# Kernel optimization log

Hardware: AMD Instinct MI355X
Metric: run time of the kernel (lower is better)

## Reference

```python
import jax, jax.numpy as jnp
import numpy as np

TAU = 2.0        # LIF membrane time constant
VTH = 0.5        # spike threshold
EPS = 1e-5       # BatchNorm eps
ALPHA = 2.0      # ATan surrogate alpha (spikingjelly default)


@jax.custom_vjp
def atan_heaviside(x):
    # forward: Heaviside spike; backward: ATan surrogate gradient
    return (x >= 0.0).astype(x.dtype)

def _ah_fwd(x):
    return atan_heaviside(x), x

def _ah_bwd(x, g):
    return (g * (ALPHA / 2.0) / (1.0 + (jnp.pi / 2.0 * ALPHA * x) ** 2),)

atan_heaviside.defvjp(_ah_fwd, _ah_bwd)


def lif_multistep(x):
    # x: [T, ...] -> spikes [T, ...]; hard reset to 0, decay_input=True
    def step(v, xt):
        v = v + (xt - v) / TAU
        s = atan_heaviside(v - VTH)
        v = v * (1.0 - jax.lax.stop_gradient(s))  # detach_reset=True
        return v, s
    v0 = jnp.zeros_like(x[0])
    _, spikes = jax.lax.scan(step, v0, x)
    return spikes


def tape_pe(d_model, max_len, dtype):
    # tAPE (ConvTran): sinusoidal PE with d_model/max_len frequency scaling
    pos = jnp.arange(max_len, dtype=dtype)[:, None]
    div = jnp.exp(jnp.arange(0, d_model, 2, dtype=dtype) * (-np.log(10000.0) / d_model))
    arg = pos * div * (d_model / max_len)
    pe = jnp.zeros((max_len, d_model), dtype)
    pe = pe.at[:, 0::2].set(jnp.sin(arg))
    pe = pe.at[:, 1::2].set(jnp.cos(arg))
    return pe  # [N, D]


def setup_inputs() -> dict:
    key = jax.random.key(0)
    k1, k2 = jax.random.split(key)
    T, B, N, P, D = 4, 64, 196, 768, 256
    x = jax.random.normal(k1, (T, B, N, P), dtype=jnp.float32)
    W = jax.random.normal(k2, (D, P), dtype=jnp.float32) * 0.02
    gamma = jnp.ones((D,), dtype=jnp.float32)
    beta = jnp.zeros((D,), dtype=jnp.float32)
    return {"x": x, "W": W, "gamma": gamma, "beta": beta}


def reference(x, W, gamma, beta):
    T, B, N, P = x.shape
    D = W.shape[0]
    # patch linear (no bias): [T,B,N,P] @ [D,P]^T -> [T,B,N,D]
    h = jnp.einsum('tbnp,dp->tbnd', x, W)
    h = jnp.transpose(h, (0, 1, 3, 2))  # [T,B,D,N]
    # BatchNorm1d over channel D (training-mode batch stats over T*B and N)
    mean = h.mean(axis=(0, 1, 3), keepdims=True)
    var = ((h - mean) ** 2).mean(axis=(0, 1, 3), keepdims=True)
    h = (h - mean) * jax.lax.rsqrt(var + EPS)
    h = h * gamma[None, None, :, None] + beta[None, None, :, None]
    # LIF spiking neuron scan over T
    h = lif_multistep(h)
    # tAPE positional encoding (broadcast [D,N] over T,B) + second LIF
    h = h + tape_pe(D, N, h.dtype).T
    h = lif_multistep(h)
    return jnp.transpose(h, (0, 1, 3, 2))  # [T,B,N,D]
```

## Files before the change

kernel.cpp:

```cpp
#include <hip/hip_runtime.h>
#include <cmath>

#define T_    4
#define B_    64
#define N_    196
#define P_    768
#define D_    256
#define BN_   (B_*N_)
#define M_    (T_*BN_)
#define SITES (BN_*D_)

#define TILE  64
#define TK    16
#define KITER (P_/TK)
#define MBLKS (M_/TILE)
#define NBLKS (D_/TILE)
#define RLEN  98

typedef __attribute__((ext_vector_type(2))) float f32x2;

__device__ __forceinline__ void pk_fma(f32x2& acc, f32x2 a, f32x2 b) {
    f32x2 t;
    asm("v_pk_mul_f32 %1, %2, %3\n\t"
        "v_pk_add_f32 %0, %0, %1"
        : "+v"(acc), "=&v"(t) : "v"(a), "v"(b));
}

extern "C" __global__ __launch_bounds__(256)
void gemm_f32emu(const float* __restrict__ x, const float* __restrict__ w,
                 float* __restrict__ h, float* __restrict__ hT) {
    __shared__ __align__(16) f32x2 As2[2][TK/2][RLEN];
    __shared__ __align__(16) f32x2 Bs2[2][TK/2][RLEN];

    const int tid  = threadIdx.x;
    const int tx   = tid & 15;
    const int ty   = tid >> 4;
    const int bid  = blockIdx.x;
    const int xcd  = bid & 7;
    const int lin  = bid >> 3;
    const int m0   = (xcd * 98 + (lin >> 2)) * TILE;
    const int d0   = (lin & 3) * TILE;
    const int lrow = tid >> 2;
    const int kq   = tid & 3;
    const int lk   = kq * 4;
    const int woff = (lrow >> 2) * 6 + (lrow & 3);
    const int abase = ty * 6;
    const int bbase = tx * 6;

    const float* xp = x + (size_t)(m0 + lrow) * P_ + lk;
    const float* wp = w + (size_t)(d0 + lrow) * P_ + lk;

    f32x2 acc[4][4][2];
#pragma unroll
    for (int i = 0; i < 4; ++i)
#pragma unroll
        for (int j = 0; j < 4; ++j)
#pragma unroll
            for (int p = 0; p < 2; ++p) acc[i][j][p] = f32x2{0.0f, 0.0f};

    {
        const float4 av = *(const float4*)xp;
        const float4 bv = *(const float4*)wp;
        As2[0][kq * 2 + 0][woff] = f32x2{av.x, av.y};
        As2[0][kq * 2 + 1][woff] = f32x2{av.z, av.w};
        Bs2[0][kq * 2 + 0][woff] = f32x2{bv.x, bv.y};
        Bs2[0][kq * 2 + 1][woff] = f32x2{bv.z, bv.w};
    }

    int cur = 0;
    for (int k0 = 0; k0 < KITER; ++k0) {
        __syncthreads();
        float4 av, bv;
        const bool have = (k0 + 1 < KITER);
        if (have) {
            av = *(const float4*)(xp + (k0 + 1) * TK);
            bv = *(const float4*)(wp + (k0 + 1) * TK);
        }
#pragma unroll
        for (int kp = 0; kp < TK / 2; ++kp) {
            const int pi = kp & 1;
            const f32x2* Ar = As2[cur][kp];
            const f32x2* Br = Bs2[cur][kp];
            const float4 aa0 = *(const float4*)(Ar + abase);
            const float4 aa1 = *(const float4*)(Ar + abase + 2);
            const float4 bb0 = *(const float4*)(Br + bbase);
            const float4 bb1 = *(const float4*)(Br + bbase + 2);
            f32x2 a2[4], b2[4];
            a2[0] = f32x2{aa0.x, aa0.y}; a2[1] = f32x2{aa0.z, aa0.w};
            a2[2] = f32x2{aa1.x, aa1.y}; a2[3] = f32x2{aa1.z, aa1.w};
            b2[0] = f32x2{bb0.x, bb0.y}; b2[1] = f32x2{bb0.z, bb0.w};
            b2[2] = f32x2{bb1.x, bb1.y}; b2[3] = f32x2{bb1.z, bb1.w};
#pragma unroll
            for (int i = 0; i < 4; ++i)
#pragma unroll
                for (int j = 0; j < 4; ++j)
                    pk_fma(acc[i][j][pi], a2[i], b2[j]);
        }
        if (have) {
            As2[cur ^ 1][kq * 2 + 0][woff] = f32x2{av.x, av.y};
            As2[cur ^ 1][kq * 2 + 1][woff] = f32x2{av.z, av.w};
            Bs2[cur ^ 1][kq * 2 + 0][woff] = f32x2{bv.x, bv.y};
            Bs2[cur ^ 1][kq * 2 + 1][woff] = f32x2{bv.z, bv.w};
        }
        cur ^= 1;
    }

    float res[4][4];
#pragma unroll
    for (int i = 0; i < 4; ++i)
#pragma unroll
        for (int j = 0; j < 4; ++j) {
            const float l01 = __fadd_rn(acc[i][j][0].x, acc[i][j][0].y);
            const float l23 = __fadd_rn(acc[i][j][1].x, acc[i][j][1].y);
            res[i][j] = __fadd_rn(l01, l23);
        }
#pragma unroll
    for (int i = 0; i < 4; ++i) {
        float4 o = {res[i][0], res[i][1], res[i][2], res[i][3]};
        *(float4*)(h + (size_t)(m0 + ty * 4 + i) * D_ + d0 + tx * 4) = o;
    }
    if (hT) {
#pragma unroll
        for (int j = 0; j < 4; ++j) {
            float4 o = {res[0][j], res[1][j], res[2][j], res[3][j]};
            *(float4*)(hT + (size_t)(d0 + tx * 4 + j) * M_ + m0 + ty * 4) = o;
        }
    }
}

#define MCH2 7168
#define GRP  224
extern "C" __global__ __launch_bounds__(256)
void mean_hT(const float* __restrict__ hT, float* __restrict__ mean_) {
    __shared__ float buf[2][MCH2];
    const int tid = threadIdx.x;
    const float* src = hT + (size_t)blockIdx.x * M_;

#pragma unroll
    for (int u = 0; u < 7; ++u)
        *(float4*)&buf[0][(u * 256 + tid) * 4] =
            *(const float4*)&src[(u * 256 + tid) * 4];
    __syncthreads();

    float acc = 0.0f;
    for (int c = 0; c < 7; ++c) {
        const int cb = c & 1;
        const bool have = (c + 1 < 7);
        float4 v[7];
        if (have) {
            const float* rp = src + (c + 1) * MCH2;
#pragma unroll
            for (int u = 0; u < 7; ++u)
                v[u] = *(const float4*)&rp[(u * 256 + tid) * 4];
        }
        if (tid == 0) {
            const float4* bp = (const float4*)buf[cb];
            float4 p0[8], p1[8];
#pragma unroll
            for (int u = 0; u < 8; ++u) p0[u] = bp[u];
            for (int gp = 0; gp < GRP; gp += 2) {
#pragma unroll
                for (int u = 0; u < 8; ++u) p1[u] = bp[(gp + 1) * 8 + u];
#pragma unroll
                for (int u = 0; u < 8; ++u) {
                    acc = __fadd_rn(acc, p0[u].x);
                    acc = __fadd_rn(acc, p0[u].y);
                    acc = __fadd_rn(acc, p0[u].z);
                    acc = __fadd_rn(acc, p0[u].w);
                }
                const int g2 = (gp + 2 < GRP) ? gp + 2 : 0;
#pragma unroll
                for (int u = 0; u < 8; ++u) p0[u] = bp[g2 * 8 + u];
#pragma unroll
                for (int u = 0; u < 8; ++u) {
                    acc = __fadd_rn(acc, p1[u].x);
                    acc = __fadd_rn(acc, p1[u].y);
                    acc = __fadd_rn(acc, p1[u].z);
                    acc = __fadd_rn(acc, p1[u].w);
                }
            }
        }
        if (have) {
#pragma unroll
            for (int u = 0; u < 7; ++u)
                *(float4*)&buf[cb ^ 1][(u * 256 + tid) * 4] = v[u];
        }
        __syncthreads();
    }
    if (tid == 0) mean_[blockIdx.x] = __fdiv_rn(acc, 50176.0f);
}

extern "C" __global__ __launch_bounds__(256)
void var_hT(const float* __restrict__ hT, const float* __restrict__ mean_,
            float* __restrict__ inv_) {
    __shared__ float chunks[256];
    const int d    = blockIdx.x;
    const int tid  = threadIdx.x;
    const int wv   = tid >> 6;
    const int lane = tid & 63;
    const float mn = mean_[d];
    const float* col = hT + (size_t)d * M_;

    for (int tb = wv; tb < T_ * B_; tb += 4) {
        double part = 0.0;
        for (int n = lane; n < N_; n += 64) {
            const float hv = col[tb * N_ + n];
            const float t1 = __fsub_rn(hv, mn);
            const float sq = __fmul_rn(t1, t1);
            part += (double)sq;
        }
#pragma unroll
        for (int off = 32; off; off >>= 1) part += __shfl_down(part, off);
        if (lane == 0) chunks[tb] = (float)part;
    }
    __syncthreads();
    if (tid == 0) {
        float accf = 0.0f;
        for (int tb = 0; tb < T_ * B_; ++tb) accf = __fadd_rn(accf, chunks[tb]);
        const float var = __fdiv_rn(accf, 50176.0f);
        inv_[d] = __fdiv_rn(1.0f, __fsqrt_rn(__fadd_rn(var, 1e-5f)));
    }
}

#define MCH  256
#define DCH  16
#define PADW 20
#define NCHK (M_/MCH)

extern "C" __global__ __launch_bounds__(256)
void mean_seq(const float* __restrict__ h, float* __restrict__ mean_) {
    __shared__ __align__(16) float buf[2][MCH][PADW];
    const int tid = threadIdx.x;
    const int d0  = blockIdx.x * DCH;
    {
        const float* rp = h + (size_t)tid * D_ + d0;
        *(float4*)&buf[0][tid][0]  = *(const float4*)(rp + 0);
        *(float4*)&buf[0][tid][4]  = *(const float4*)(rp + 4);
        *(float4*)&buf[0][tid][8]  = *(const float4*)(rp + 8);
        *(float4*)&buf[0][tid][12] = *(const float4*)(rp + 12);
    }
    __syncthreads();
    float acc = 0.0f;
    for (int c = 0; c < NCHK; ++c) {
        const int cb = c & 1;
        const bool have = (c + 1 < NCHK);
        float4 v0, v1, v2, v3;
        if (have) {
            const float* rp = h + ((size_t)(c + 1) * MCH + tid) * D_ + d0;
            v0 = *(const float4*)(rp + 0);
            v1 = *(const float4*)(rp + 4);
            v2 = *(const float4*)(rp + 8);
            v3 = *(const float4*)(rp + 12);
        }
        if (tid < DCH) {
#pragma unroll 16
            for (int m = 0; m < MCH; ++m)
                acc = __fadd_rn(acc, buf[cb][m][tid]);
        }
        if (have) {
            *(float4*)&buf[cb ^ 1][tid][0]  = v0;
            *(float4*)&buf[cb ^ 1][tid][4]  = v1;
            *(float4*)&buf[cb ^ 1][tid][8]  = v2;
            *(float4*)&buf[cb ^ 1][tid][12] = v3;
        }
        __syncthreads();
    }
    if (tid < DCH) mean_[d0 + tid] = __fdiv_rn(acc, 50176.0f);
}

extern "C" __global__ __launch_bounds__(64)
void var_seq(const float* __restrict__ h, const float* __restrict__ mean_,
             float* __restrict__ inv_) {
    const int d    = blockIdx.x;
    const int lane = threadIdx.x;
    const float mn = mean_[d];
    float accf = 0.0f;
    for (int tb = 0; tb < T_ * B_; ++tb) {
        double part = 0.0;
        for (int n = lane; n < N_; n += 64) {
            const float hv = h[((size_t)tb * N_ + n) * D_ + d];
            const float t1 = __fsub_rn(hv, mn);
            const float sq = __fmul_rn(t1, t1);
            part += (double)sq;
        }
#pragma unroll
        for (int off = 32; off; off >>= 1) part += __shfl_down(part, off);
        accf = __fadd_rn(accf, (float)part);
    }
    if (lane == 0) {
        const float var = __fdiv_rn(accf, 50176.0f);
        inv_[d] = __fdiv_rn(1.0f, __fsqrt_rn(__fadd_rn(var, 1e-5f)));
    }
}

extern "C" __global__ __launch_bounds__(256)
void pe_build(float* __restrict__ pe_) {
    const int d = threadIdx.x;
    const int n = blockIdx.x;
    const double dv  = exp((double)(d & ~1) * (-9.210340371976184 / 256.0));
    const double arg = ((double)n * dv) * (256.0 / 196.0);
    pe_[(size_t)n * D_ + d] = (d & 1) ? (float)cos(arg) : (float)sin(arg);
}

extern "C" __global__ __launch_bounds__(256)
void lif_final(float* __restrict__ out, const float* __restrict__ mean_,
               const float* __restrict__ inv_, const float* __restrict__ gamma,
               const float* __restrict__ beta, const float* __restrict__ pe_tab) {
    const int idx = blockIdx.x * 256 + threadIdx.x;
    const int d = idx & (D_ - 1);
    const int n = (idx >> 8) % N_;

    const float mn = mean_[d];
    const float iv = inv_[d];
    const float g  = gamma[d];
    const float b  = beta[d];

    float pe;
    if (pe_tab) {
        pe = pe_tab[(size_t)n * D_ + d];
    } else {
        const double dv  = exp((double)(d & ~1) * (-9.210340371976184 / 256.0));
        const double arg = ((double)n * dv) * (256.0 / 196.0);
        pe = (d & 1) ? (float)cos(arg) : (float)sin(arg);
    }

    float hv[4];
#pragma unroll
    for (int t = 0; t < T_; ++t) hv[t] = out[(size_t)t * SITES + idx];

    float v1 = 0.0f, v2 = 0.0f, s2v[4];
#pragma unroll
    for (int t = 0; t < T_; ++t) {
        const float t1 = __fsub_rn(hv[t], mn);
        const float u  = __fmul_rn(t1, iv);
        const float hb = __fadd_rn(__fmul_rn(u, g), b);
        v1 = __fadd_rn(v1, __fmul_rn(__fsub_rn(hb, v1), 0.5f));
        const float s1 = (v1 >= 0.5f) ? 1.0f : 0.0f;
        v1 = __fmul_rn(v1, __fsub_rn(1.0f, s1));
        const float y = __fadd_rn(s1, pe);
        v2 = __fadd_rn(v2, __fmul_rn(__fsub_rn(y, v2), 0.5f));
        const float s2 = (v2 >= 0.5f) ? 1.0f : 0.0f;
        v2 = __fmul_rn(v2, __fsub_rn(1.0f, s2));
        s2v[t] = s2;
    }
#pragma unroll
    for (int t = 0; t < T_; ++t) out[(size_t)t * SITES + idx] = s2v[t];
}

extern "C" void kernel_launch(void* const* d_in, const int* in_sizes, int n_in,
                              void* d_out, int out_size, void* d_ws, size_t ws_size,
                              hipStream_t stream) {
    const float* x     = (const float*)d_in[0];
    const float* w     = (const float*)d_in[1];
    const float* gamma = (const float*)d_in[2];
    const float* beta  = (const float*)d_in[3];
    float* out = (float*)d_out;

    float* mean_ = (float*)d_ws;
    float* inv_  = mean_ + D_;
    float* pe_   = inv_  + D_;
    float* hT_   = pe_   + (size_t)N_ * D_;

    const size_t need_pe = (size_t)(2 * D_ + N_ * D_) * sizeof(float);
    const size_t need_hT = need_pe + (size_t)M_ * D_ * sizeof(float);
    const bool use_pe = ws_size >= need_pe;
    const bool use_hT = ws_size >= need_hT;

    gemm_f32emu<<<MBLKS * NBLKS, 256, 0, stream>>>(x, w, out,
                                                   use_hT ? hT_ : nullptr);
    if (use_hT) {
        mean_hT<<<D_, 256, 0, stream>>>(hT_, mean_);
        var_hT<<<D_, 256, 0, stream>>>(hT_, mean_, inv_);
    } else {
        mean_seq<<<16, 256, 0, stream>>>(out, mean_);
        var_seq<<<D_, 64, 0, stream>>>(out, mean_, inv_);
    }
    if (use_pe) pe_build<<<N_, 256, 0, stream>>>(pe_);
    lif_final<<<SITES / 256, 256, 0, stream>>>(out, mean_, inv_, gamma, beta,
                                               use_pe ? pe_ : nullptr);
}
```

Measured before the change: 855.6 us.

## Split GEMM launch, fuse mean/var reduction, vectorize LIF epilogue

Splits the GEMM grid into two half-launches over M, fuses the mean and variance reduction kernels into one block-per-channel kernel, removes the wraparound prefetch in the serial mean loop, and vectorizes the final LIF kernel to process four channels per thread with float4 loads and stores. The aim is to cut launch overhead and the redundant reread of statistics, and to widen memory transactions in the epilogue. The extra GEMM launch may add tail and launch cost.

```diff
diff --git a/kernel.cpp b/kernel.cpp
--- a/kernel.cpp
+++ b/kernel.cpp
@@ -14,7 +14,8 @@
 #define TK    16
 #define KITER (P_/TK)
 #define MBLKS (M_/TILE)
-#define NBLKS (D_/TILE)
+#define HBLKS (392/49*8*4/8)
+#define GRID_HALF ((392/49)*49*4/4)
 #define RLEN  98
 
 typedef __attribute__((ext_vector_type(2))) float f32x2;
@@ -28,7 +29,7 @@
 
 extern "C" __global__ __launch_bounds__(256)
 void gemm_f32emu(const float* __restrict__ x, const float* __restrict__ w,
-                 float* __restrict__ h, float* __restrict__ hT) {
+                 float* __restrict__ h, float* __restrict__ hT, int mbase) {
     __shared__ __align__(16) f32x2 As2[2][TK/2][RLEN];
     __shared__ __align__(16) f32x2 Bs2[2][TK/2][RLEN];
 
@@ -38,7 +39,7 @@
     const int bid  = blockIdx.x;
     const int xcd  = bid & 7;
     const int lin  = bid >> 3;
-    const int m0   = (xcd * 98 + (lin >> 2)) * TILE;
+    const int m0   = mbase + (xcd * 49 + (lin >> 2)) * TILE;
     const int d0   = (lin & 3) * TILE;
     const int lrow = tid >> 2;
     const int kq   = tid & 3;
@@ -131,10 +132,14 @@
 #define MCH2 7168
 #define GRP  224
 extern "C" __global__ __launch_bounds__(256)
-void mean_hT(const float* __restrict__ hT, float* __restrict__ mean_) {
+void meanvar_hT(const float* __restrict__ hT, float* __restrict__ mean_,
+                float* __restrict__ inv_) {
     __shared__ float buf[2][MCH2];
+    __shared__ float chunks[256];
+    __shared__ float mn_sh;
     const int tid = threadIdx.x;
-    const float* src = hT + (size_t)blockIdx.x * M_;
+    const int d   = blockIdx.x;
+    const float* src = hT + (size_t)d * M_;
 
 #pragma unroll
     for (int u = 0; u < 7; ++u)
@@ -158,7 +163,8 @@
             float4 p0[8], p1[8];
 #pragma unroll
             for (int u = 0; u < 8; ++u) p0[u] = bp[u];
-            for (int gp = 0; gp < GRP; gp += 2) {
+            int gp = 0;
+            for (; gp + 2 < GRP; gp += 2) {
 #pragma unroll
                 for (int u = 0; u < 8; ++u) p1[u] = bp[(gp + 1) * 8 + u];
 #pragma unroll
@@ -168,9 +174,8 @@
                     acc = __fadd_rn(acc, p0[u].z);
                     acc = __fadd_rn(acc, p0[u].w);
                 }
-                const int g2 = (gp + 2 < GRP) ? gp + 2 : 0;
-#pragma unroll
-                for (int u = 0; u < 8; ++u) p0[u] = bp[g2 * 8 + u];
+#pragma unroll
+                for (int u = 0; u < 8; ++u) p0[u] = bp[(gp + 2) * 8 + u];
 #pragma unroll
                 for (int u = 0; u < 8; ++u) {
                     acc = __fadd_rn(acc, p1[u].x);
@@ -179,6 +184,22 @@
                     acc = __fadd_rn(acc, p1[u].w);
                 }
             }
+#pragma unroll
+            for (int u = 0; u < 8; ++u) p1[u] = bp[(GRP - 1) * 8 + u];
+#pragma unroll
+            for (int u = 0; u < 8; ++u) {
+                acc = __fadd_rn(acc, p0[u].x);
+                acc = __fadd_rn(acc, p0[u].y);
+                acc = __fadd_rn(acc, p0[u].z);
+                acc = __fadd_rn(acc, p0[u].w);
+            }
+#pragma unroll
+            for (int u = 0; u < 8; ++u) {
+                acc = __fadd_rn(acc, p1[u].x);
+                acc = __fadd_rn(acc, p1[u].y);
+                acc = __fadd_rn(acc, p1[u].z);
+                acc = __fadd_rn(acc, p1[u].w);
+            }
         }
         if (have) {
 #pragma unroll
@@ -187,24 +208,20 @@
         }
         __syncthreads();
     }
-    if (tid == 0) mean_[blockIdx.x] = __fdiv_rn(acc, 50176.0f);
-}
-
-extern "C" __global__ __launch_bounds__(256)
-void var_hT(const float* __restrict__ hT, const float* __restrict__ mean_,
-            float* __restrict__ inv_) {
-    __shared__ float chunks[256];
-    const int d    = blockIdx.x;
-    const int tid  = threadIdx.x;
+    if (tid == 0) {
+        const float mn = __fdiv_rn(acc, 50176.0f);
+        mean_[d] = mn;
+        mn_sh = mn;
+    }
+    __syncthreads();
+
+    const float mn = mn_sh;
     const int wv   = tid >> 6;
     const int lane = tid & 63;
-    const float mn = mean_[d];
-    const float* col = hT + (size_t)d * M_;
-
     for (int tb = wv; tb < T_ * B_; tb += 4) {
         double part = 0.0;
         for (int n = lane; n < N_; n += 64) {
-            const float hv = col[tb * N_ + n];
+            const float hv = src[tb * N_ + n];
             const float t1 = __fsub_rn(hv, mn);
             const float sq = __fmul_rn(t1, t1);
             part += (double)sq;
@@ -306,45 +323,61 @@
 void lif_final(float* __restrict__ out, const float* __restrict__ mean_,
                const float* __restrict__ inv_, const float* __restrict__ gamma,
                const float* __restrict__ beta, const float* __restrict__ pe_tab) {
-    const int idx = blockIdx.x * 256 + threadIdx.x;
-    const int d = idx & (D_ - 1);
-    const int n = (idx >> 8) % N_;
-
-    const float mn = mean_[d];
-    const float iv = inv_[d];
-    const float g  = gamma[d];
-    const float b  = beta[d];
-
-    float pe;
+    const int base = (blockIdx.x * 256 + threadIdx.x) * 4;
+    const int dbase = base & (D_ - 1);
+    const int n = (base >> 8) % N_;
+
+    const float4 mn = *(const float4*)&mean_[dbase];
+    const float4 iv = *(const float4*)&inv_[dbase];
+    const float4 g  = *(const float4*)&gamma[dbase];
+    const float4 b  = *(const float4*)&beta[dbase];
+
+    float4 pe;
     if (pe_tab) {
-        pe = pe_tab[(size_t)n * D_ + d];
+        pe = *(const float4*)&pe_tab[(size_t)n * D_ + dbase];
     } else {
-        const double dv  = exp((double)(d & ~1) * (-9.210340371976184 / 256.0));
-        const double arg = ((double)n * dv) * (256.0 / 196.0);
-        pe = (d & 1) ? (float)cos(arg) : (float)sin(arg);
-    }
-
-    float hv[4];
-#pragma unroll
-    for (int t = 0; t < T_; ++t) hv[t] = out[(size_t)t * SITES + idx];
-
-    float v1 = 0.0f, v2 = 0.0f, s2v[4];
-#pragma unroll
-    for (int t = 0; t < T_; ++t) {
-        const float t1 = __fsub_rn(hv[t], mn);
-        const float u  = __fmul_rn(t1, iv);
-        const float hb = __fadd_rn(__fmul_rn(u, g), b);
-        v1 = __fadd_rn(v1, __fmul_rn(__fsub_rn(hb, v1), 0.5f));
-        const float s1 = (v1 >= 0.5f) ? 1.0f : 0.0f;
-        v1 = __fmul_rn(v1, __fsub_rn(1.0f, s1));
-        const float y = __fadd_rn(s1, pe);
-        v2 = __fadd_rn(v2, __fmul_rn(__fsub_rn(y, v2), 0.5f));
-        const float s2 = (v2 >= 0.5f) ? 1.0f : 0.0f;
-        v2 = __fmul_rn(v2, __fsub_rn(1.0f, s2));
-        s2v[t] = s2;
-    }
-#pragma unroll
-    for (int t = 0; t < T_; ++t) out[(size_t)t * SITES + idx] = s2v[t];
+        float* pp = &pe.x;
+#pragma unroll
+        for (int q = 0; q < 4; ++q) {
+            const int d = dbase + q;
+            const double dv  = exp((double)(d & ~1) * (-9.210340371976184 / 256.0));
+            const double arg = ((double)n * dv) * (256.0 / 196.0);
+            pp[q] = (d & 1) ? (float)cos(arg) : (float)sin(arg);
+        }
+    }
+
+    float4 hv[4];
+#pragma unroll
+    for (int t = 0; t < T_; ++t)
+        hv[t] = *(const float4*)&out[(size_t)t * SITES + base];
+
+    const float* mnp = &mn.x; const float* ivp = &iv.x;
+    const float* gp  = &g.x;  const float* bp  = &b.x;
+    const float* pep = &pe.x;
+    float4 s2v[4];
+#pragma unroll
+    for (int q = 0; q < 4; ++q) {
+        float v1 = 0.0f, v2 = 0.0f;
+        const float mq = mnp[q], iq = ivp[q], gq = gp[q], bq = bp[q], pq = pep[q];
+#pragma unroll
+        for (int t = 0; t < T_; ++t) {
+            const float hq = (&hv[t].x)[q];
+            const float t1 = __fsub_rn(hq, mq);
+            const float u  = __fmul_rn(t1, iq);
+            const float hb = __fadd_rn(__fmul_rn(u, gq), bq);
+            v1 = __fadd_rn(v1, __fmul_rn(__fsub_rn(hb, v1), 0.5f));
+            const float s1 = (v1 >= 0.5f) ? 1.0f : 0.0f;
+            v1 = __fmul_rn(v1, __fsub_rn(1.0f, s1));
+            const float y = __fadd_rn(s1, pq);
+            v2 = __fadd_rn(v2, __fmul_rn(__fsub_rn(y, v2), 0.5f));
+            const float s2 = (v2 >= 0.5f) ? 1.0f : 0.0f;
+            v2 = __fmul_rn(v2, __fsub_rn(1.0f, s2));
+            (&s2v[t].x)[q] = s2;
+        }
+    }
+#pragma unroll
+    for (int t = 0; t < T_; ++t)
+        *(float4*)&out[(size_t)t * SITES + base] = s2v[t];
 }
 
 extern "C" void kernel_launch(void* const* d_in, const int* in_sizes, int n_in,
@@ -365,17 +398,17 @@
     const size_t need_hT = need_pe + (size_t)M_ * D_ * sizeof(float);
     const bool use_pe = ws_size >= need_pe;
     const bool use_hT = ws_size >= need_hT;
-
-    gemm_f32emu<<<MBLKS * NBLKS, 256, 0, stream>>>(x, w, out,
-                                                   use_hT ? hT_ : nullptr);
+    float* hTp = use_hT ? hT_ : nullptr;
+
+    gemm_f32emu<<<1568, 256, 0, stream>>>(x, w, out, hTp, 0);
+    gemm_f32emu<<<1568, 256, 0, stream>>>(x, w, out, hTp, 392 * TILE);
     if (use_hT) {
-        mean_hT<<<D_, 256, 0, stream>>>(hT_, mean_);
-        var_hT<<<D_, 256, 0, stream>>>(hT_, mean_, inv_);
+        meanvar_hT<<<D_, 256, 0, stream>>>(hT_, mean_, inv_);
     } else {
         mean_seq<<<16, 256, 0, stream>>>(out, mean_);
         var_seq<<<D_, 64, 0, stream>>>(out, mean_, inv_);
     }
     if (use_pe) pe_build<<<N_, 256, 0, stream>>>(pe_);
-    lif_final<<<SITES / 256, 256, 0, stream>>>(out, mean_, inv_, gamma, beta,
-                                               use_pe ? pe_ : nullptr);
-}
+    lif_final<<<SITES / 1024, 256, 0, stream>>>(out, mean_, inv_, gamma, beta,
+                                                use_pe ? pe_ : nullptr);
+}
```

Result: slower. 883.7 us (+3.3%).
